# Kernel optimization log

Hardware: AMD Instinct MI355X
Metric: run time of the kernel (lower is better)

Reference implementation:

```python
import jax, jax.numpy as jnp
import numpy as np

EPS_SQRT = 1e-9
EPS_NORM = 1e-12


def setup_inputs() -> dict:
    key = jax.random.key(0)
    k1, k2 = jax.random.split(key)
    shape = (32, 112, 112, 128)  # B, H, W, C
    left = jax.random.normal(k1, shape, dtype=jnp.float32)
    right = jax.random.normal(k2, shape, dtype=jnp.float32)
    return {"left": left, "right": right}


def reference(left, right):
    B, H, W, C = left.shape
    # reshape to [B, H*W, C] and contract over the spatial dim -> [B, C, C]
    l = left.reshape(B, H * W, C)
    r = right.reshape(B, H * W, C)
    dotted = jnp.einsum('bxc,bxd->bcd', l, r)  # batched outer-product pooling
    flat = dotted.reshape(B, C * C)
    # signed square root
    sqrted = jnp.sign(flat) * jnp.sqrt(jnp.abs(flat) + EPS_SQRT)
    # L2 normalize over the flattened bilinear vector (tf.math.l2_normalize)
    sumsq = jnp.sum(jnp.square(sqrted), axis=-1, keepdims=True)
    normed = sqrted * jax.lax.rsqrt(jnp.maximum(sumsq, EPS_NORM))
    return normed
```

## Files before the change

kernel.cpp:

```cpp
#include <hip/hip_runtime.h>
#include <hip/hip_bf16.h>


#define NK      8
#define KC      1568
#define BK      32
#define NT      49
#define BATCH   32
#define CDIM    128
#define XDIM    12544

typedef __bf16 bf16x8 __attribute__((ext_vector_type(8)));
typedef float  f32x16 __attribute__((ext_vector_type(16)));

__device__ float g_part[(size_t)NK * BATCH * CDIM * CDIM];
__device__ float g_ssq[BATCH * 16];

__device__ __forceinline__ void split8(const float* f, uint4& hi, uint4& lo) {
  uint xh[8], xl[8];
#pragma unroll
  for (int i = 0; i < 8; ++i) {
    uint u = __float_as_uint(f[i]);
    uint r = u + 0x7FFFu + ((u >> 16) & 1u);
    xh[i] = r;
    float hif = __uint_as_float(r & 0xFFFF0000u);
    xl[i] = __float_as_uint(f[i] - hif);
  }
  hi.x = __builtin_amdgcn_perm(xh[1], xh[0], 0x07060302u);
  hi.y = __builtin_amdgcn_perm(xh[3], xh[2], 0x07060302u);
  hi.z = __builtin_amdgcn_perm(xh[5], xh[4], 0x07060302u);
  hi.w = __builtin_amdgcn_perm(xh[7], xh[6], 0x07060302u);
  lo.x = __builtin_amdgcn_perm(xl[1], xl[0], 0x07060302u);
  lo.y = __builtin_amdgcn_perm(xl[3], xl[2], 0x07060302u);
  lo.z = __builtin_amdgcn_perm(xl[5], xl[4], 0x07060302u);
  lo.w = __builtin_amdgcn_perm(xl[7], xl[6], 0x07060302u);
}

__device__ __forceinline__ int ldsu(int c, int kh) {
  return ((c << 1) | kh) ^ ((c >> 2) & 7);
}

__global__ __launch_bounds__(512, 2)
void bcnn_gemm_kernel(const float* __restrict__ L, const float* __restrict__ R) {
  __shared__ uint4 sAhi[2][2][256], sAlo[2][2][256];
  __shared__ uint4 sBhi[2][2][256], sBlo[2][2][256];

  const int chunk = blockIdx.x;
  const int b     = blockIdx.y;
  const int t     = threadIdx.x;
  const int l     = t & 63;
  const int w     = t >> 6;
  const int wr    = w >> 2;
  const int wc    = w & 3;
  const int lc    = l & 31;
  const int hh    = l >> 5;

  const int sc  = t & 127;
  const int sh  = t >> 7;
  const int sub = sh >> 1;
  const int wu  = ldsu(sc, sh & 1);

  const float* gL = L + ((size_t)b * XDIM + (size_t)chunk * KC + sh * 8) * CDIM + sc;
  const float* gR = R + ((size_t)b * XDIM + (size_t)chunk * KC + sh * 8) * CDIM + sc;

  const int cA0 = wr * 64 + lc;
  const int cA1 = cA0 + 32;
  const int dB  = wc * 32 + lc;
  const int uA0 = ldsu(cA0, hh);
  const int uA1 = ldsu(cA1, hh);
  const int uB  = ldsu(dB,  hh);

  f32x16 acc0 = {};
  f32x16 acc1 = {};

  float rlA[8], rrA[8], rlB[8], rrB[8], rlC[8], rrC[8];

#define LOADR(rl, rr, s)                                                        \
  do {                                                                          \
    const float* pL_ = gL + (size_t)(s) * BK * CDIM;                            \
    const float* pR_ = gR + (size_t)(s) * BK * CDIM;                            \
    _Pragma("unroll")                                                           \
    for (int i = 0; i < 8; ++i) { rl[i] = pL_[i * CDIM]; rr[i] = pR_[i * CDIM]; } \
  } while (0)

#define WRITE(rl, rr, set)                                                      \
  do {                                                                          \
    uint4 hi_, lo_;                                                             \
    split8(rl, hi_, lo_);                                                       \
    sAhi[set][sub][wu] = hi_; sAlo[set][sub][wu] = lo_;                         \
    split8(rr, hi_, lo_);                                                       \
    sBhi[set][sub][wu] = hi_; sBlo[set][sub][wu] = lo_;                         \
  } while (0)

#define COMPUTE(set)                                                            \
  do {                                                                          \
    _Pragma("unroll")                                                           \
    for (int ss = 0; ss < 2; ++ss) {                                            \
      bf16x8 ah0 = *(const bf16x8*)&sAhi[set][ss][uA0];                         \
      bf16x8 al0 = *(const bf16x8*)&sAlo[set][ss][uA0];                         \
      bf16x8 ah1 = *(const bf16x8*)&sAhi[set][ss][uA1];                         \
      bf16x8 al1 = *(const bf16x8*)&sAlo[set][ss][uA1];                         \
      bf16x8 bh  = *(const bf16x8*)&sBhi[set][ss][uB];                          \
      bf16x8 bl  = *(const bf16x8*)&sBlo[set][ss][uB];                          \
      acc0 = __builtin_amdgcn_mfma_f32_32x32x16_bf16(ah0, bh, acc0, 0, 0, 0);   \
      acc1 = __builtin_amdgcn_mfma_f32_32x32x16_bf16(ah1, bh, acc1, 0, 0, 0);   \
      acc0 = __builtin_amdgcn_mfma_f32_32x32x16_bf16(ah0, bl, acc0, 0, 0, 0);   \
      acc1 = __builtin_amdgcn_mfma_f32_32x32x16_bf16(ah1, bl, acc1, 0, 0, 0);   \
      acc0 = __builtin_amdgcn_mfma_f32_32x32x16_bf16(al0, bh, acc0, 0, 0, 0);   \
      acc1 = __builtin_amdgcn_mfma_f32_32x32x16_bf16(al1, bh, acc1, 0, 0, 0);   \
    }                                                                           \
  } while (0)

#define BAR()                                                                   \
  do {                                                                          \
    asm volatile("s_waitcnt lgkmcnt(0)" ::: "memory");                          \
    __builtin_amdgcn_s_barrier();                                               \
  } while (0)

  LOADR(rlA, rrA, 0);
  LOADR(rlB, rrB, 1);
  LOADR(rlC, rrC, 2);
  WRITE(rlA, rrA, 0);
  BAR();

  for (int it = 0; it < 7; ++it) {
    const int s0 = 6 * it;
     LOADR(rlA, rrA, s0 + 3); COMPUTE(0); WRITE(rlB, rrB, 1); BAR();
     LOADR(rlB, rrB, s0 + 4); COMPUTE(1); WRITE(rlC, rrC, 0); BAR();
     LOADR(rlC, rrC, s0 + 5); COMPUTE(0); WRITE(rlA, rrA, 1); BAR();
     LOADR(rlA, rrA, s0 + 6); COMPUTE(1); WRITE(rlB, rrB, 0); BAR();
     LOADR(rlB, rrB, s0 + 7); COMPUTE(0); WRITE(rlC, rrC, 1); BAR();
     LOADR(rlC, rrC, s0 + 8); COMPUTE(1); WRITE(rlA, rrA, 0); BAR();
  }
   LOADR(rlA, rrA, 45); COMPUTE(0); WRITE(rlB, rrB, 1); BAR();
   LOADR(rlB, rrB, 46); COMPUTE(1); WRITE(rlC, rrC, 0); BAR();
   LOADR(rlC, rrC, 47); COMPUTE(0); WRITE(rlA, rrA, 1); BAR();
   LOADR(rlA, rrA, 48); COMPUTE(1); WRITE(rlB, rrB, 0); BAR();
   COMPUTE(0); WRITE(rlC, rrC, 1); BAR();
   COMPUTE(1); WRITE(rlA, rrA, 0); BAR();
   COMPUTE(0);

#undef LOADR
#undef WRITE
#undef COMPUTE
#undef BAR

  float* outp = g_part + (((size_t)chunk * BATCH + b) << 14);
#pragma unroll
  for (int r = 0; r < 16; ++r) {
    const int row = (r & 3) + ((r >> 2) << 3) + (hh << 2);
    outp[(size_t)(wr * 64 + row) * CDIM + (wc * 32 + lc)]      = acc0[r];
    outp[(size_t)(wr * 64 + 32 + row) * CDIM + (wc * 32 + lc)] = acc1[r];
  }
}

__global__ void bcnn_sqrt_kernel(float* __restrict__ out) {
  const int b   = blockIdx.y;
  const int seg = blockIdx.x;
  const int t   = threadIdx.x;
  const int idx = seg * 1024 + t * 4;

  float4 v = {0.f, 0.f, 0.f, 0.f};
#pragma unroll
  for (int ch = 0; ch < NK; ++ch) {
    const float4 p = *(const float4*)&g_part[(((size_t)ch * BATCH + b) << 14) + idx];
    v.x += p.x; v.y += p.y; v.z += p.z; v.w += p.w;
  }
  float4 sv;
  {
    float a;
    a = sqrtf(fabsf(v.x) + 1e-9f); sv.x = (v.x > 0.f) ? a : ((v.x < 0.f) ? -a : 0.f);
    a = sqrtf(fabsf(v.y) + 1e-9f); sv.y = (v.y > 0.f) ? a : ((v.y < 0.f) ? -a : 0.f);
    a = sqrtf(fabsf(v.z) + 1e-9f); sv.z = (v.z > 0.f) ? a : ((v.z < 0.f) ? -a : 0.f);
    a = sqrtf(fabsf(v.w) + 1e-9f); sv.w = (v.w > 0.f) ? a : ((v.w < 0.f) ? -a : 0.f);
  }
  *(float4*)&out[((size_t)b << 14) + idx] = sv;

  float ss = sv.x * sv.x + sv.y * sv.y + sv.z * sv.z + sv.w * sv.w;
#pragma unroll
  for (int o = 32; o > 0; o >>= 1) ss += __shfl_down(ss, o, 64);
  __shared__ float red[4];
  if ((t & 63) == 0) red[t >> 6] = ss;
  __syncthreads();
  if (t == 0) g_ssq[b * 16 + seg] = red[0] + red[1] + red[2] + red[3];
}

__global__ void bcnn_scale_kernel(float* __restrict__ out) {
  const int b   = blockIdx.y;
  const int seg = blockIdx.x;
  const int t   = threadIdx.x;

  float tot = 0.f;
#pragma unroll
  for (int i = 0; i < 16; ++i) tot += g_ssq[b * 16 + i];
  const float scale = rsqrtf(fmaxf(tot, 1e-12f));

  const size_t base = ((size_t)b << 14) + seg * 1024 + t * 4;
  float4 v = *(float4*)&out[base];
  v.x *= scale; v.y *= scale; v.z *= scale; v.w *= scale;
  *(float4*)&out[base] = v;
}

extern "C" void kernel_launch(void* const* d_in, const int* in_sizes, int n_in,
                              void* d_out, int out_size, void* d_ws, size_t ws_size,
                              hipStream_t stream) {
  const float* L = (const float*)d_in[0];
  const float* R = (const float*)d_in[1];
  float* out = (float*)d_out;

  dim3 g1(NK, BATCH);
  bcnn_gemm_kernel<<<g1, 512, 0, stream>>>(L, R);

  dim3 g2(16, BATCH);
  bcnn_sqrt_kernel<<<g2, 256, 0, stream>>>(out);
  bcnn_scale_kernel<<<g2, 256, 0, stream>>>(out);
}
```

Before: 87.99 us.

## Split K across warp groups with 64x64 warp tiles and LDS reduction

Each warp now computes a 64x64 output tile (four accumulators) on one K sub-slice, instead of a 64x32 tile over both sub-slices. This raises MFMA work per LDS fragment load, cutting LDS read traffic per MFMA. The two K-halves are summed through shared memory at the end before the partial results are written out. The cost is doubled accumulator registers, which may pressure occupancy at 2 blocks per CU, plus an extra reduction phase.

```diff
diff --git a/kernel.cpp b/kernel.cpp
--- a/kernel.cpp
+++ b/kernel.cpp
@@ -40,38 +40,38 @@
   return ((c << 1) | kh) ^ ((c >> 2) & 7);
 }
 
+#define REGN(set, sub, mat, hilo) (((((((set)*2 + (sub))*2 + (mat))*2) + (hilo)) * 256))
+
 __global__ __launch_bounds__(512, 2)
 void bcnn_gemm_kernel(const float* __restrict__ L, const float* __restrict__ R) {
-  __shared__ uint4 sAhi[2][2][256], sAlo[2][2][256];
-  __shared__ uint4 sBhi[2][2][256], sBlo[2][2][256];
+  __shared__ uint4 smem[4096];
 
   const int chunk = blockIdx.x;
   const int b     = blockIdx.y;
   const int t     = threadIdx.x;
   const int l     = t & 63;
   const int w     = t >> 6;
-  const int wr    = w >> 2;
-  const int wc    = w & 3;
   const int lc    = l & 31;
   const int hh    = l >> 5;
-
-  const int sc  = t & 127;
-  const int sh  = t >> 7;
-  const int sub = sh >> 1;
-  const int wu  = ldsu(sc, sh & 1);
+  const int sub   = w >> 2;
+  const int q     = w & 3;
+  const int qr    = q >> 1;
+  const int qc    = q & 1;
+
+  const int sc   = t & 127;
+  const int sh   = t >> 7;
+  const int ssub = sh >> 1;
+  const int wu   = ldsu(sc, sh & 1);
 
   const float* gL = L + ((size_t)b * XDIM + (size_t)chunk * KC + sh * 8) * CDIM + sc;
   const float* gR = R + ((size_t)b * XDIM + (size_t)chunk * KC + sh * 8) * CDIM + sc;
 
-  const int cA0 = wr * 64 + lc;
-  const int cA1 = cA0 + 32;
-  const int dB  = wc * 32 + lc;
-  const int uA0 = ldsu(cA0, hh);
-  const int uA1 = ldsu(cA1, hh);
-  const int uB  = ldsu(dB,  hh);
-
-  f32x16 acc0 = {};
-  f32x16 acc1 = {};
+  const int uA0 = ldsu(qr * 64 + lc,      hh);
+  const int uA1 = ldsu(qr * 64 + 32 + lc, hh);
+  const int uB0 = ldsu(qc * 64 + lc,      hh);
+  const int uB1 = ldsu(qc * 64 + 32 + lc, hh);
+
+  f32x16 acc00 = {}, acc01 = {}, acc10 = {}, acc11 = {};
 
   float rlA[8], rrA[8], rlB[8], rrB[8], rlC[8], rrC[8];
 
@@ -87,28 +87,35 @@
   do {                                                                          \
     uint4 hi_, lo_;                                                             \
     split8(rl, hi_, lo_);                                                       \
-    sAhi[set][sub][wu] = hi_; sAlo[set][sub][wu] = lo_;                         \
+    smem[REGN(set, ssub, 0, 0) + wu] = hi_;                                     \
+    smem[REGN(set, ssub, 0, 1) + wu] = lo_;                                     \
     split8(rr, hi_, lo_);                                                       \
-    sBhi[set][sub][wu] = hi_; sBlo[set][sub][wu] = lo_;                         \
+    smem[REGN(set, ssub, 1, 0) + wu] = hi_;                                     \
+    smem[REGN(set, ssub, 1, 1) + wu] = lo_;                                     \
   } while (0)
 
 #define COMPUTE(set)                                                            \
   do {                                                                          \
-    _Pragma("unroll")                                                           \
-    for (int ss = 0; ss < 2; ++ss) {                                            \
-      bf16x8 ah0 = *(const bf16x8*)&sAhi[set][ss][uA0];                         \
-      bf16x8 al0 = *(const bf16x8*)&sAlo[set][ss][uA0];                         \
-      bf16x8 ah1 = *(const bf16x8*)&sAhi[set][ss][uA1];                         \
-      bf16x8 al1 = *(const bf16x8*)&sAlo[set][ss][uA1];                         \
-      bf16x8 bh  = *(const bf16x8*)&sBhi[set][ss][uB];                          \
-      bf16x8 bl  = *(const bf16x8*)&sBlo[set][ss][uB];                          \
-      acc0 = __builtin_amdgcn_mfma_f32_32x32x16_bf16(ah0, bh, acc0, 0, 0, 0);   \
-      acc1 = __builtin_amdgcn_mfma_f32_32x32x16_bf16(ah1, bh, acc1, 0, 0, 0);   \
-      acc0 = __builtin_amdgcn_mfma_f32_32x32x16_bf16(ah0, bl, acc0, 0, 0, 0);   \
-      acc1 = __builtin_amdgcn_mfma_f32_32x32x16_bf16(ah1, bl, acc1, 0, 0, 0);   \
-      acc0 = __builtin_amdgcn_mfma_f32_32x32x16_bf16(al0, bh, acc0, 0, 0, 0);   \
-      acc1 = __builtin_amdgcn_mfma_f32_32x32x16_bf16(al1, bh, acc1, 0, 0, 0);   \
-    }                                                                           \
+    bf16x8 ah0 = *(const bf16x8*)&smem[REGN(set, sub, 0, 0) + uA0];             \
+    bf16x8 al0 = *(const bf16x8*)&smem[REGN(set, sub, 0, 1) + uA0];             \
+    bf16x8 ah1 = *(const bf16x8*)&smem[REGN(set, sub, 0, 0) + uA1];             \
+    bf16x8 al1 = *(const bf16x8*)&smem[REGN(set, sub, 0, 1) + uA1];             \
+    bf16x8 bh0 = *(const bf16x8*)&smem[REGN(set, sub, 1, 0) + uB0];             \
+    bf16x8 bl0 = *(const bf16x8*)&smem[REGN(set, sub, 1, 1) + uB0];             \
+    bf16x8 bh1 = *(const bf16x8*)&smem[REGN(set, sub, 1, 0) + uB1];             \
+    bf16x8 bl1 = *(const bf16x8*)&smem[REGN(set, sub, 1, 1) + uB1];             \
+    acc00 = __builtin_amdgcn_mfma_f32_32x32x16_bf16(ah0, bh0, acc00, 0, 0, 0);  \
+    acc01 = __builtin_amdgcn_mfma_f32_32x32x16_bf16(ah0, bh1, acc01, 0, 0, 0);  \
+    acc10 = __builtin_amdgcn_mfma_f32_32x32x16_bf16(ah1, bh0, acc10, 0, 0, 0);  \
+    acc11 = __builtin_amdgcn_mfma_f32_32x32x16_bf16(ah1, bh1, acc11, 0, 0, 0);  \
+    acc00 = __builtin_amdgcn_mfma_f32_32x32x16_bf16(ah0, bl0, acc00, 0, 0, 0);  \
+    acc01 = __builtin_amdgcn_mfma_f32_32x32x16_bf16(ah0, bl1, acc01, 0, 0, 0);  \
+    acc10 = __builtin_amdgcn_mfma_f32_32x32x16_bf16(ah1, bl0, acc10, 0, 0, 0);  \
+    acc11 = __builtin_amdgcn_mfma_f32_32x32x16_bf16(ah1, bl1, acc11, 0, 0, 0);  \
+    acc00 = __builtin_amdgcn_mfma_f32_32x32x16_bf16(al0, bh0, acc00, 0, 0, 0);  \
+    acc01 = __builtin_amdgcn_mfma_f32_32x32x16_bf16(al0, bh1, acc01, 0, 0, 0);  \
+    acc10 = __builtin_amdgcn_mfma_f32_32x32x16_bf16(al1, bh0, acc10, 0, 0, 0);  \
+    acc11 = __builtin_amdgcn_mfma_f32_32x32x16_bf16(al1, bh1, acc11, 0, 0, 0);  \
   } while (0)
 
 #define BAR()                                                                   \
@@ -143,15 +150,42 @@
 #undef LOADR
 #undef WRITE
 #undef COMPUTE
+
+  BAR();
+  float* fs = (float*)smem;
+  if (w >= 4) {
+    const int base = (w - 4) * 4096 + l;
+#pragma unroll
+    for (int r = 0; r < 16; ++r) {
+      fs[base +    0 + r * 64] = acc00[r];
+      fs[base + 1024 + r * 64] = acc01[r];
+      fs[base + 2048 + r * 64] = acc10[r];
+      fs[base + 3072 + r * 64] = acc11[r];
+    }
+  }
+  BAR();
+  if (w < 4) {
+    const int base = w * 4096 + l;
+#pragma unroll
+    for (int r = 0; r < 16; ++r) {
+      acc00[r] += fs[base +    0 + r * 64];
+      acc01[r] += fs[base + 1024 + r * 64];
+      acc10[r] += fs[base + 2048 + r * 64];
+      acc11[r] += fs[base + 3072 + r * 64];
+    }
+    float* outp = g_part + (((size_t)chunk * BATCH + b) << 14);
+#pragma unroll
+    for (int r = 0; r < 16; ++r) {
+      const int row = (r & 3) + ((r >> 2) << 3) + (hh << 2);
+      const int r0 = qr * 64 + row;
+      const int c0 = qc * 64 + lc;
+      outp[(size_t)(r0)      * CDIM + c0]      = acc00[r];
+      outp[(size_t)(r0)      * CDIM + c0 + 32] = acc01[r];
+      outp[(size_t)(r0 + 32) * CDIM + c0]      = acc10[r];
+      outp[(size_t)(r0 + 32) * CDIM + c0 + 32] = acc11[r];
+    }
+  }
 #undef BAR
-
-  float* outp = g_part + (((size_t)chunk * BATCH + b) << 14);
-#pragma unroll
-  for (int r = 0; r < 16; ++r) {
-    const int row = (r & 3) + ((r >> 2) << 3) + (hh << 2);
-    outp[(size_t)(wr * 64 + row) * CDIM + (wc * 32 + lc)]      = acc0[r];
-    outp[(size_t)(wr * 64 + 32 + row) * CDIM + (wc * 32 + lc)] = acc1[r];
-  }
 }
 
 __global__ void bcnn_sqrt_kernel(float* __restrict__ out) {
```

Result: slower. 92.32 us (+4.9%).

## Double GEMM block to 1024 threads with one 32x32 tile per wave

Applied to the files above, without the earlier changes.

The GEMM kernel goes from 512 to 1024 threads per block. Each of the 16 waves now owns a single 32x32 output tile instead of two, and each thread loads and splits 4 rows instead of 8. Shared memory is packed into one array, and writes use uint2 halves so that two threads fill each 16-byte slot. This raises the number of waves per CU to hide memory latency, but each wave loses the reuse of its B fragment across two MFMA tiles, so LDS read traffic per MFMA goes up.

```diff
diff --git a/kernel.cpp b/kernel.cpp
--- a/kernel.cpp
+++ b/kernel.cpp
@@ -16,10 +16,10 @@
 __device__ float g_part[(size_t)NK * BATCH * CDIM * CDIM];
 __device__ float g_ssq[BATCH * 16];
 
-__device__ __forceinline__ void split8(const float* f, uint4& hi, uint4& lo) {
-  uint xh[8], xl[8];
-#pragma unroll
-  for (int i = 0; i < 8; ++i) {
+__device__ __forceinline__ void split4(const float* f, uint2& hi, uint2& lo) {
+  uint xh[4], xl[4];
+#pragma unroll
+  for (int i = 0; i < 4; ++i) {
     uint u = __float_as_uint(f[i]);
     uint r = u + 0x7FFFu + ((u >> 16) & 1u);
     xh[i] = r;
@@ -28,22 +28,19 @@
   }
   hi.x = __builtin_amdgcn_perm(xh[1], xh[0], 0x07060302u);
   hi.y = __builtin_amdgcn_perm(xh[3], xh[2], 0x07060302u);
-  hi.z = __builtin_amdgcn_perm(xh[5], xh[4], 0x07060302u);
-  hi.w = __builtin_amdgcn_perm(xh[7], xh[6], 0x07060302u);
   lo.x = __builtin_amdgcn_perm(xl[1], xl[0], 0x07060302u);
   lo.y = __builtin_amdgcn_perm(xl[3], xl[2], 0x07060302u);
-  lo.z = __builtin_amdgcn_perm(xl[5], xl[4], 0x07060302u);
-  lo.w = __builtin_amdgcn_perm(xl[7], xl[6], 0x07060302u);
 }
 
 __device__ __forceinline__ int ldsu(int c, int kh) {
   return ((c << 1) | kh) ^ ((c >> 2) & 7);
 }
 
-__global__ __launch_bounds__(512, 2)
+#define REGN(set, sub, mat, hilo) ((((((set)*2 + (sub))*2 + (mat))*2) + (hilo)) * 256)
+
+__global__ __launch_bounds__(1024, 4)
 void bcnn_gemm_kernel(const float* __restrict__ L, const float* __restrict__ R) {
-  __shared__ uint4 sAhi[2][2][256], sAlo[2][2][256];
-  __shared__ uint4 sBhi[2][2][256], sBlo[2][2][256];
+  __shared__ uint4 smem[4096];
 
   const int chunk = blockIdx.x;
   const int b     = blockIdx.y;
@@ -55,59 +52,53 @@
   const int lc    = l & 31;
   const int hh    = l >> 5;
 
-  const int sc  = t & 127;
-  const int sh  = t >> 7;
-  const int sub = sh >> 1;
-  const int wu  = ldsu(sc, sh & 1);
-
-  const float* gL = L + ((size_t)b * XDIM + (size_t)chunk * KC + sh * 8) * CDIM + sc;
-  const float* gR = R + ((size_t)b * XDIM + (size_t)chunk * KC + sh * 8) * CDIM + sc;
-
-  const int cA0 = wr * 64 + lc;
-  const int cA1 = cA0 + 32;
-  const int dB  = wc * 32 + lc;
-  const int uA0 = ldsu(cA0, hh);
-  const int uA1 = ldsu(cA1, hh);
-  const int uB  = ldsu(dB,  hh);
-
-  f32x16 acc0 = {};
-  f32x16 acc1 = {};
-
-  float rlA[8], rrA[8], rlB[8], rrB[8], rlC[8], rrC[8];
+  const int sc   = t & 127;
+  const int sh   = t >> 7;
+  const int ssub = sh >> 2;
+  const int khs  = (sh >> 1) & 1;
+  const int half = sh & 1;
+  const int wu   = ldsu(sc, khs);
+
+  const float* gL = L + ((size_t)b * XDIM + (size_t)chunk * KC + sh * 4) * CDIM + sc;
+  const float* gR = R + ((size_t)b * XDIM + (size_t)chunk * KC + sh * 4) * CDIM + sc;
+
+  const int uA = ldsu(wr * 32 + lc, hh);
+  const int uB = ldsu(wc * 32 + lc, hh);
+
+  f32x16 acc = {};
+
+  float rlA[4], rrA[4], rlB[4], rrB[4], rlC[4], rrC[4];
 
 #define LOADR(rl, rr, s)                                                        \
   do {                                                                          \
     const float* pL_ = gL + (size_t)(s) * BK * CDIM;                            \
     const float* pR_ = gR + (size_t)(s) * BK * CDIM;                            \
     _Pragma("unroll")                                                           \
-    for (int i = 0; i < 8; ++i) { rl[i] = pL_[i * CDIM]; rr[i] = pR_[i * CDIM]; } \
+    for (int i = 0; i < 4; ++i) { rl[i] = pL_[i * CDIM]; rr[i] = pR_[i * CDIM]; } \
   } while (0)
 
 #define WRITE(rl, rr, set)                                                      \
   do {                                                                          \
-    uint4 hi_, lo_;                                                             \
-    split8(rl, hi_, lo_);                                                       \
-    sAhi[set][sub][wu] = hi_; sAlo[set][sub][wu] = lo_;                         \
-    split8(rr, hi_, lo_);                                                       \
-    sBhi[set][sub][wu] = hi_; sBlo[set][sub][wu] = lo_;                         \
+    uint2 hi_, lo_;                                                             \
+    split4(rl, hi_, lo_);                                                       \
+    ((uint2*)smem)[(REGN(set, ssub, 0, 0) + wu) * 2 + half] = hi_;              \
+    ((uint2*)smem)[(REGN(set, ssub, 0, 1) + wu) * 2 + half] = lo_;              \
+    split4(rr, hi_, lo_);                                                       \
+    ((uint2*)smem)[(REGN(set, ssub, 1, 0) + wu) * 2 + half] = hi_;              \
+    ((uint2*)smem)[(REGN(set, ssub, 1, 1) + wu) * 2 + half] = lo_;              \
   } while (0)
 
 #define COMPUTE(set)                                                            \
   do {                                                                          \
     _Pragma("unroll")                                                           \
     for (int ss = 0; ss < 2; ++ss) {                                            \
-      bf16x8 ah0 = *(const bf16x8*)&sAhi[set][ss][uA0];                         \
-      bf16x8 al0 = *(const bf16x8*)&sAlo[set][ss][uA0];                         \
-      bf16x8 ah1 = *(const bf16x8*)&sAhi[set][ss][uA1];                         \
-      bf16x8 al1 = *(const bf16x8*)&sAlo[set][ss][uA1];                         \
-      bf16x8 bh  = *(const bf16x8*)&sBhi[set][ss][uB];                          \
-      bf16x8 bl  = *(const bf16x8*)&sBlo[set][ss][uB];                          \
-      acc0 = __builtin_amdgcn_mfma_f32_32x32x16_bf16(ah0, bh, acc0, 0, 0, 0);   \
-      acc1 = __builtin_amdgcn_mfma_f32_32x32x16_bf16(ah1, bh, acc1, 0, 0, 0);   \
-      acc0 = __builtin_amdgcn_mfma_f32_32x32x16_bf16(ah0, bl, acc0, 0, 0, 0);   \
-      acc1 = __builtin_amdgcn_mfma_f32_32x32x16_bf16(ah1, bl, acc1, 0, 0, 0);   \
-      acc0 = __builtin_amdgcn_mfma_f32_32x32x16_bf16(al0, bh, acc0, 0, 0, 0);   \
-      acc1 = __builtin_amdgcn_mfma_f32_32x32x16_bf16(al1, bh, acc1, 0, 0, 0);   \
+      bf16x8 ah = *(const bf16x8*)&smem[REGN(set, ss, 0, 0) + uA];              \
+      bf16x8 al = *(const bf16x8*)&smem[REGN(set, ss, 0, 1) + uA];              \
+      bf16x8 bh = *(const bf16x8*)&smem[REGN(set, ss, 1, 0) + uB];              \
+      bf16x8 bl = *(const bf16x8*)&smem[REGN(set, ss, 1, 1) + uB];              \
+      acc = __builtin_amdgcn_mfma_f32_32x32x16_bf16(ah, bh, acc, 0, 0, 0);      \
+      acc = __builtin_amdgcn_mfma_f32_32x32x16_bf16(ah, bl, acc, 0, 0, 0);      \
+      acc = __builtin_amdgcn_mfma_f32_32x32x16_bf16(al, bh, acc, 0, 0, 0);      \
     }                                                                           \
   } while (0)
 
@@ -149,8 +140,7 @@
 #pragma unroll
   for (int r = 0; r < 16; ++r) {
     const int row = (r & 3) + ((r >> 2) << 3) + (hh << 2);
-    outp[(size_t)(wr * 64 + row) * CDIM + (wc * 32 + lc)]      = acc0[r];
-    outp[(size_t)(wr * 64 + 32 + row) * CDIM + (wc * 32 + lc)] = acc1[r];
+    outp[(size_t)(wr * 32 + row) * CDIM + (wc * 32 + lc)] = acc[r];
   }
 }
 
@@ -209,7 +199,7 @@
   float* out = (float*)d_out;
 
   dim3 g1(NK, BATCH);
-  bcnn_gemm_kernel<<<g1, 512, 0, stream>>>(L, R);
+  bcnn_gemm_kernel<<<g1, 1024, 0, stream>>>(L, R);
 
   dim3 g2(16, BATCH);
   bcnn_sqrt_kernel<<<g2, 256, 0, stream>>>(out);
```

Result: no change. 88.99 us (+1.1%).
